# Performance work log

Hardware: AMD Instinct MI355X
Metric: run time of the kernel (lower is better)

The kernel has to match this reference:

```python
import jax, jax.numpy as jnp
import numpy as np

SEQ, D_IN, D_OUT = 8192, 1024, 1024

def setup_inputs() -> dict:
    key = jax.random.key(0)
    kx, kq, kk, kv = jax.random.split(key, 4)
    scale = 1.0 / np.sqrt(D_IN)
    return {
        "x": jax.random.normal(kx, (SEQ, D_IN), dtype=jnp.float32),
        "Wq": jax.random.normal(kq, (D_OUT, D_IN), dtype=jnp.float32) * scale,
        "Wk": jax.random.normal(kk, (D_OUT, D_IN), dtype=jnp.float32) * scale,
        "Wv": jax.random.normal(kv, (D_OUT, D_IN), dtype=jnp.float32) * scale,
    }

def reference(x, Wq, Wk, Wv):
    # nn.Linear: y = x @ W.T (no bias)
    q = x @ Wq.T            # [S, d_out]
    k = x @ Wk.T            # [S, d_out]
    v = x @ Wv.T            # [S, d_out]
    d_k = k.shape[-1]
    scores = (q @ k.T) / jnp.sqrt(jnp.float32(d_k))   # [S, S]
    attn = jax.nn.softmax(scores, axis=-1)
    return attn @ v         # [S, d_out]
```

## Files before the change

kernel.cpp:

```cpp
#include <hip/hip_runtime.h>

typedef unsigned short ushort_t;
typedef __bf16 bf16_t;
typedef __attribute__((ext_vector_type(8))) __bf16 bf16x8;
typedef __attribute__((ext_vector_type(4))) float f32x4;

#define SEQ 8192
#define DIN 1024
#define DOUT 1024

__device__ __forceinline__ ushort_t f2bf(float f) {
  union { float f; unsigned u; } c; c.f = f;
  unsigned u = c.u;
  return (ushort_t)((u + 0x7fffu + ((u >> 16) & 1u)) >> 16);
}
__device__ __forceinline__ float bf2f(ushort_t h) {
  union { unsigned u; float f; } c; c.u = ((unsigned)h) << 16;
  return c.f;
}

__device__ __forceinline__ void async16(ushort_t* lds, const ushort_t* g) {
  __builtin_amdgcn_global_load_lds(
      (__attribute__((address_space(1))) void*)g,
      (__attribute__((address_space(3))) void*)lds, 16, 0, 0);
}

__global__ __launch_bounds__(256) void cvt_kernel(const float* __restrict__ in,
                                                  ushort_t* __restrict__ out, int n4) {
  int i = blockIdx.x * 256 + threadIdx.x;
  if (i >= n4) return;
  float4 f = ((const float4*)in)[i];
  ushort4 o;
  o.x = f2bf(f.x); o.y = f2bf(f.y); o.z = f2bf(f.z); o.w = f2bf(f.w);
  ((ushort4*)out)[i] = o;
}

__global__ __launch_bounds__(256) void transpose_kernel(const ushort_t* __restrict__ in,
                                                        ushort_t* __restrict__ out,
                                                        int rows, int cols) {
  __shared__ ushort_t tile[32][33];
  int tx = threadIdx.x & 31, ty = threadIdx.x >> 5;
  int r0 = blockIdx.y * 32, c0 = blockIdx.x * 32;
  #pragma unroll
  for (int i = 0; i < 32; i += 8)
    tile[ty + i][tx] = in[(size_t)(r0 + ty + i) * cols + c0 + tx];
  __syncthreads();
  #pragma unroll
  for (int i = 0; i < 32; i += 8)
    out[(size_t)(c0 + ty + i) * rows + r0 + tx] = tile[tx][ty + i];
}

template <bool F32OUT>
__global__ __launch_bounds__(256) void gemm_bt(const ushort_t* __restrict__ A,
                                               const ushort_t* __restrict__ B,
                                               void* __restrict__ C,
                                               int M, int N, int K, float scale) {
  __shared__ ushort_t As[128 * 64];
  __shared__ ushort_t Bs[128 * 64];
  const int t = threadIdx.x;
  const int lane = t & 63;
  const int wave = t >> 6;
  const int wr = wave >> 1, wc = wave & 1;
  const int quad = lane >> 4, r16 = lane & 15;
  const int rowBase = blockIdx.y * 128;
  const int colBase = blockIdx.x * 128;

  f32x4 acc[4][4] = {};

  const int nk = K >> 6;
  for (int kt = 0; kt < nk; ++kt) {
    #pragma unroll
    for (int i = 0; i < 4; ++i) {
      int c = t + i * 256;
      int row = c >> 3;
      int kq = (c & 7) ^ (row & 7);
      async16(&As[c * 8], A + (size_t)(rowBase + row) * K + kt * 64 + kq * 8);
      async16(&Bs[c * 8], B + (size_t)(colBase + row) * K + kt * 64 + kq * 8);
    }
    __syncthreads();
    #pragma unroll
    for (int ks = 0; ks < 2; ++ks) {
      bf16x8 af[4], bfr[4];
      #pragma unroll
      for (int mi = 0; mi < 4; ++mi) {
        int row = wr * 64 + mi * 16 + r16;
        int kq = ks * 4 + quad;
        int c = (row << 3) | (kq ^ (row & 7));
        af[mi] = *(const bf16x8*)&As[c * 8];
      }
      #pragma unroll
      for (int ni = 0; ni < 4; ++ni) {
        int row = wc * 64 + ni * 16 + r16;
        int kq = ks * 4 + quad;
        int c = (row << 3) | (kq ^ (row & 7));
        bfr[ni] = *(const bf16x8*)&Bs[c * 8];
      }
      #pragma unroll
      for (int mi = 0; mi < 4; ++mi)
        #pragma unroll
        for (int ni = 0; ni < 4; ++ni)
          acc[mi][ni] = __builtin_amdgcn_mfma_f32_16x16x32_bf16(af[mi], bfr[ni],
                                                                acc[mi][ni], 0, 0, 0);
    }
    __syncthreads();
  }

  #pragma unroll
  for (int mi = 0; mi < 4; ++mi)
    #pragma unroll
    for (int ni = 0; ni < 4; ++ni)
      #pragma unroll
      for (int r = 0; r < 4; ++r) {
        int grow = rowBase + wr * 64 + mi * 16 + quad * 4 + r;
        int gcol = colBase + wc * 64 + ni * 16 + r16;
        float v = acc[mi][ni][r] * scale;
        if (F32OUT)
          ((float*)C)[(size_t)grow * N + gcol] = v;
        else
          ((ushort_t*)C)[(size_t)grow * N + gcol] = f2bf(v);
      }
}

__global__ __launch_bounds__(256) void softmax_kernel(ushort_t* __restrict__ S) {
  ushort_t* row = S + (size_t)blockIdx.x * SEQ;
  const int t = threadIdx.x;
  __shared__ float red[8];
  float v[32];
  float m = -1e30f;
  #pragma unroll
  for (int i = 0; i < 32; ++i) {
    v[i] = bf2f(row[t + i * 256]);
    m = fmaxf(m, v[i]);
  }
  #pragma unroll
  for (int off = 32; off >= 1; off >>= 1) m = fmaxf(m, __shfl_xor(m, off, 64));
  if ((t & 63) == 0) red[t >> 6] = m;
  __syncthreads();
  m = fmaxf(fmaxf(red[0], red[1]), fmaxf(red[2], red[3]));
  float s = 0.f;
  #pragma unroll
  for (int i = 0; i < 32; ++i) {
    v[i] = __expf(v[i] - m);
    s += v[i];
  }
  #pragma unroll
  for (int off = 32; off >= 1; off >>= 1) s += __shfl_xor(s, off, 64);
  if ((t & 63) == 0) red[4 + (t >> 6)] = s;
  __syncthreads();
  s = red[4] + red[5] + red[6] + red[7];
  float inv = 1.0f / s;
  #pragma unroll
  for (int i = 0; i < 32; ++i) row[t + i * 256] = f2bf(v[i] * inv);
}

extern "C" void kernel_launch(void* const* d_in, const int* in_sizes, int n_in,
                              void* d_out, int out_size, void* d_ws, size_t ws_size,
                              hipStream_t stream) {
  const float* x  = (const float*)d_in[0];
  const float* Wq = (const float*)d_in[1];
  const float* Wk = (const float*)d_in[2];
  const float* Wv = (const float*)d_in[3];
  float* out = (float*)d_out;

  char* p = (char*)d_ws;
  ushort_t* xb  = (ushort_t*)p; p += (size_t)SEQ * DIN * 2;
  ushort_t* wqb = (ushort_t*)p; p += (size_t)DOUT * DIN * 2;
  ushort_t* wkb = (ushort_t*)p; p += (size_t)DOUT * DIN * 2;
  ushort_t* wvb = (ushort_t*)p; p += (size_t)DOUT * DIN * 2;
  ushort_t* qb  = (ushort_t*)p; p += (size_t)SEQ * DOUT * 2;
  ushort_t* kb  = (ushort_t*)p; p += (size_t)SEQ * DOUT * 2;
  ushort_t* vb  = (ushort_t*)p; p += (size_t)SEQ * DOUT * 2;
  ushort_t* vtb = (ushort_t*)p; p += (size_t)SEQ * DOUT * 2;
  ushort_t* Sb  = (ushort_t*)p; p += (size_t)SEQ * SEQ * 2;

  int n4x = SEQ * DIN / 4;
  cvt_kernel<<<(n4x + 255) / 256, 256, 0, stream>>>(x, xb, n4x);
  int n4w = DOUT * DIN / 4;
  cvt_kernel<<<(n4w + 255) / 256, 256, 0, stream>>>(Wq, wqb, n4w);
  cvt_kernel<<<(n4w + 255) / 256, 256, 0, stream>>>(Wk, wkb, n4w);
  cvt_kernel<<<(n4w + 255) / 256, 256, 0, stream>>>(Wv, wvb, n4w);

  dim3 blk(256);
  dim3 g1(DOUT / 128, SEQ / 128);
  gemm_bt<false><<<g1, blk, 0, stream>>>(xb, wqb, qb, SEQ, DOUT, DIN, 1.0f);
  gemm_bt<false><<<g1, blk, 0, stream>>>(xb, wkb, kb, SEQ, DOUT, DIN, 1.0f);
  gemm_bt<false><<<g1, blk, 0, stream>>>(xb, wvb, vb, SEQ, DOUT, DIN, 1.0f);

  transpose_kernel<<<dim3(DOUT / 32, SEQ / 32), blk, 0, stream>>>(vb, vtb, SEQ, DOUT);

  dim3 g2(SEQ / 128, SEQ / 128);
  gemm_bt<false><<<g2, blk, 0, stream>>>(qb, kb, Sb, SEQ, SEQ, DIN, 0.03125f);

  softmax_kernel<<<SEQ, blk, 0, stream>>>(Sb);

  dim3 g3(DOUT / 128, SEQ / 128);
  gemm_bt<true><<<g3, blk, 0, stream>>>(Sb, vtb, out, SEQ, DOUT, SEQ, 1.0f);
}
```

Measured before the change: 540.0 us.

## Fuse QK projection, compute V transposed directly, merge converts, swizzle PV tiles

```diff
diff --git a/kernel.cpp b/kernel.cpp
--- a/kernel.cpp
+++ b/kernel.cpp
@@ -1,7 +1,6 @@
 #include <hip/hip_runtime.h>
 
 typedef unsigned short ushort_t;
-typedef __bf16 bf16_t;
 typedef __attribute__((ext_vector_type(8))) __bf16 bf16x8;
 typedef __attribute__((ext_vector_type(4))) float f32x4;
 
@@ -25,36 +24,37 @@
       (__attribute__((address_space(3))) void*)lds, 16, 0, 0);
 }
 
-__global__ __launch_bounds__(256) void cvt_kernel(const float* __restrict__ in,
-                                                  ushort_t* __restrict__ out, int n4) {
-  int i = blockIdx.x * 256 + threadIdx.x;
-  if (i >= n4) return;
-  float4 f = ((const float4*)in)[i];
+__global__ __launch_bounds__(256) void cvt_all_kernel(
+    const float* __restrict__ x, const float* __restrict__ wq,
+    const float* __restrict__ wk, const float* __restrict__ wv,
+    ushort_t* __restrict__ xb, ushort_t* __restrict__ wqkb,
+    ushort_t* __restrict__ wvb) {
+  int b = blockIdx.x;
+  const float* src;
+  ushort_t* dst;
+  int idx;
+  if (b < 8192) {
+    src = x; dst = xb; idx = b * 256 + threadIdx.x;
+  } else {
+    int r = b - 8192;
+    int w = r >> 10;
+    idx = (r & 1023) * 256 + threadIdx.x;
+    if (w == 0)      { src = wq; dst = wqkb; }
+    else if (w == 1) { src = wk; dst = wqkb + DOUT * DIN; }
+    else             { src = wv; dst = wvb; }
+  }
+  float4 f = ((const float4*)src)[idx];
   ushort4 o;
   o.x = f2bf(f.x); o.y = f2bf(f.y); o.z = f2bf(f.z); o.w = f2bf(f.w);
-  ((ushort4*)out)[i] = o;
+  ((ushort4*)dst)[idx] = o;
 }
 
-__global__ __launch_bounds__(256) void transpose_kernel(const ushort_t* __restrict__ in,
-                                                        ushort_t* __restrict__ out,
-                                                        int rows, int cols) {
-  __shared__ ushort_t tile[32][33];
-  int tx = threadIdx.x & 31, ty = threadIdx.x >> 5;
-  int r0 = blockIdx.y * 32, c0 = blockIdx.x * 32;
-  #pragma unroll
-  for (int i = 0; i < 32; i += 8)
-    tile[ty + i][tx] = in[(size_t)(r0 + ty + i) * cols + c0 + tx];
-  __syncthreads();
-  #pragma unroll
-  for (int i = 0; i < 32; i += 8)
-    out[(size_t)(c0 + ty + i) * rows + r0 + tx] = tile[tx][ty + i];
-}
-
-template <bool F32OUT>
+template <bool F32OUT, bool SWZ>
 __global__ __launch_bounds__(256) void gemm_bt(const ushort_t* __restrict__ A,
                                                const ushort_t* __restrict__ B,
                                                void* __restrict__ C,
-                                               int M, int N, int K, float scale) {
+                                               int lda, int ldb, int ldc,
+                                               int K, float scale) {
   __shared__ ushort_t As[128 * 64];
   __shared__ ushort_t Bs[128 * 64];
   const int t = threadIdx.x;
@@ -62,8 +62,17 @@
   const int wave = t >> 6;
   const int wr = wave >> 1, wc = wave & 1;
   const int quad = lane >> 4, r16 = lane & 15;
-  const int rowBase = blockIdx.y * 128;
-  const int colBase = blockIdx.x * 128;
+
+  int mt, nt;
+  if (SWZ) {
+    mt = blockIdx.x * (gridDim.y >> 3) + (blockIdx.y >> 3);
+    nt = blockIdx.y & 7;
+  } else {
+    mt = blockIdx.y;
+    nt = blockIdx.x;
+  }
+  const int rowBase = mt * 128;
+  const int colBase = nt * 128;
 
   f32x4 acc[4][4] = {};
 
@@ -74,8 +83,8 @@
       int c = t + i * 256;
       int row = c >> 3;
       int kq = (c & 7) ^ (row & 7);
-      async16(&As[c * 8], A + (size_t)(rowBase + row) * K + kt * 64 + kq * 8);
-      async16(&Bs[c * 8], B + (size_t)(colBase + row) * K + kt * 64 + kq * 8);
+      async16(&As[c * 8], A + (size_t)(rowBase + row) * lda + kt * 64 + kq * 8);
+      async16(&Bs[c * 8], B + (size_t)(colBase + row) * ldb + kt * 64 + kq * 8);
     }
     __syncthreads();
     #pragma unroll
@@ -115,9 +124,9 @@
         int gcol = colBase + wc * 64 + ni * 16 + r16;
         float v = acc[mi][ni][r] * scale;
         if (F32OUT)
-          ((float*)C)[(size_t)grow * N + gcol] = v;
+          ((float*)C)[(size_t)grow * ldc + gcol] = v;
         else
-          ((ushort_t*)C)[(size_t)grow * N + gcol] = f2bf(v);
+          ((ushort_t*)C)[(size_t)grow * ldc + gcol] = f2bf(v);
       }
 }
 
@@ -163,36 +172,27 @@
   float* out = (float*)d_out;
 
   char* p = (char*)d_ws;
-  ushort_t* xb  = (ushort_t*)p; p += (size_t)SEQ * DIN * 2;
-  ushort_t* wqb = (ushort_t*)p; p += (size_t)DOUT * DIN * 2;
-  ushort_t* wkb = (ushort_t*)p; p += (size_t)DOUT * DIN * 2;
-  ushort_t* wvb = (ushort_t*)p; p += (size_t)DOUT * DIN * 2;
-  ushort_t* qb  = (ushort_t*)p; p += (size_t)SEQ * DOUT * 2;
-  ushort_t* kb  = (ushort_t*)p; p += (size_t)SEQ * DOUT * 2;
-  ushort_t* vb  = (ushort_t*)p; p += (size_t)SEQ * DOUT * 2;
-  ushort_t* vtb = (ushort_t*)p; p += (size_t)SEQ * DOUT * 2;
-  ushort_t* Sb  = (ushort_t*)p; p += (size_t)SEQ * SEQ * 2;
+  ushort_t* xb   = (ushort_t*)p; p += (size_t)SEQ * DIN * 2;
+  ushort_t* wqkb = (ushort_t*)p; p += (size_t)2 * DOUT * DIN * 2;
+  ushort_t* wvb  = (ushort_t*)p; p += (size_t)DOUT * DIN * 2;
+  ushort_t* qkb  = (ushort_t*)p; p += (size_t)SEQ * 2 * DOUT * 2;
+  ushort_t* vtb  = (ushort_t*)p; p += (size_t)DOUT * SEQ * 2;
+  ushort_t* Sb   = (ushort_t*)p; p += (size_t)SEQ * SEQ * 2;
 
-  int n4x = SEQ * DIN / 4;
-  cvt_kernel<<<(n4x + 255) / 256, 256, 0, stream>>>(x, xb, n4x);
-  int n4w = DOUT * DIN / 4;
-  cvt_kernel<<<(n4w + 255) / 256, 256, 0, stream>>>(Wq, wqb, n4w);
-  cvt_kernel<<<(n4w + 255) / 256, 256, 0, stream>>>(Wk, wkb, n4w);
-  cvt_kernel<<<(n4w + 255) / 256, 256, 0, stream>>>(Wv, wvb, n4w);
+  cvt_all_kernel<<<8192 + 3 * 1024, 256, 0, stream>>>(x, Wq, Wk, Wv, xb, wqkb, wvb);
 
   dim3 blk(256);
-  dim3 g1(DOUT / 128, SEQ / 128);
-  gemm_bt<false><<<g1, blk, 0, stream>>>(xb, wqb, qb, SEQ, DOUT, DIN, 1.0f);
-  gemm_bt<false><<<g1, blk, 0, stream>>>(xb, wkb, kb, SEQ, DOUT, DIN, 1.0f);
-  gemm_bt<false><<<g1, blk, 0, stream>>>(xb, wvb, vb, SEQ, DOUT, DIN, 1.0f);
+  gemm_bt<false, false><<<dim3(2048 / 128, SEQ / 128), blk, 0, stream>>>(
+      xb, wqkb, qkb, DIN, DIN, 2 * DOUT, DIN, 1.0f);
 
-  transpose_kernel<<<dim3(DOUT / 32, SEQ / 32), blk, 0, stream>>>(vb, vtb, SEQ, DOUT);
+  gemm_bt<false, false><<<dim3(SEQ / 128, DOUT / 128), blk, 0, stream>>>(
+      wvb, xb, vtb, DIN, DIN, SEQ, DIN, 1.0f);
 
-  dim3 g2(SEQ / 128, SEQ / 128);
-  gemm_bt<false><<<g2, blk, 0, stream>>>(qb, kb, Sb, SEQ, SEQ, DIN, 0.03125f);
+  gemm_bt<false, false><<<dim3(SEQ / 128, SEQ / 128), blk, 0, stream>>>(
+      qkb, qkb + DOUT, Sb, 2 * DOUT, 2 * DOUT, SEQ, DIN, 0.03125f);
 
   softmax_kernel<<<SEQ, blk, 0, stream>>>(Sb);
 
-  dim3 g3(DOUT / 128, SEQ / 128);
-  gemm_bt<true><<<g3, blk, 0, stream>>>(Sb, vtb, out, SEQ, DOUT, SEQ, 1.0f);
+  gemm_bt<true, true><<<dim3(DOUT / 128, SEQ / 128), blk, 0, stream>>>(
+      Sb, vtb, out, SEQ, SEQ, DOUT, SEQ, 1.0f);
 }
```

Result: faster. 503.6 us (-6.7%).
